# Kernel optimization log

Measured on AMD Instinct MI355X. Metric: run time of the kernel, lower is better.

## Reference

```python
import jax, jax.numpy as jnp
import numpy as np

N_NODES = 50000
N_EDGES = 200000


def _glorot(key, shape):
    fan_in, fan_out = shape[0], shape[1]
    lim = np.sqrt(6.0 / (fan_in + fan_out))
    return jax.random.uniform(key, shape, jnp.float32, -lim, lim)


def setup_inputs() -> dict:
    key = jax.random.key(0)
    ks = jax.random.split(key, 20)
    x = jax.random.normal(ks[0], (N_NODES, 2), jnp.float32)
    edge_index = jax.random.randint(ks[1], (2, N_EDGES), 0, N_NODES, jnp.int64)
    edge_attr = jax.random.uniform(ks[2], (N_EDGES, 2), jnp.float32)
    # conv1: NNConv(2 -> 32), edge nn: Linear(2,16) -> ReLU -> Linear(16, 2*32)
    nn1_w1 = _glorot(ks[3], (2, 16)); nn1_b1 = jnp.zeros((16,), jnp.float32)
    nn1_w2 = _glorot(ks[4], (16, 64)); nn1_b2 = jnp.zeros((64,), jnp.float32)
    root1 = _glorot(ks[5], (2, 32)); bias1 = jnp.zeros((32,), jnp.float32)
    # conv2: NNConv(32 -> 32), edge nn: Linear(2,16) -> ReLU -> Linear(16, 1024)
    nn2_w1 = _glorot(ks[6], (2, 16)); nn2_b1 = jnp.zeros((16,), jnp.float32)
    nn2_w2 = _glorot(ks[7], (16, 1024)); nn2_b2 = jnp.zeros((1024,), jnp.float32)
    root2 = _glorot(ks[8], (32, 32)); bias2 = jnp.zeros((32,), jnp.float32)
    # fc2: Linear(32 -> 1)  (fc1 is unused in the original forward)
    fc2_w = _glorot(ks[9], (32, 1)); fc2_b = jnp.zeros((1,), jnp.float32)
    return dict(x=x, edge_index=edge_index, edge_attr=edge_attr,
                nn1_w1=nn1_w1, nn1_b1=nn1_b1, nn1_w2=nn1_w2, nn1_b2=nn1_b2,
                root1=root1, bias1=bias1,
                nn2_w1=nn2_w1, nn2_b1=nn2_b1, nn2_w2=nn2_w2, nn2_b2=nn2_b2,
                root2=root2, bias2=bias2, fc2_w=fc2_w, fc2_b=fc2_b)


def _nnconv(x, src, dst, edge_attr, w1, b1, w2, b2, root, bias, in_ch, out_ch):
    # per-edge weight matrices from edge MLP: [E, in_ch*out_ch]
    h = jax.nn.relu(edge_attr @ w1 + b1) @ w2 + b2
    W = h.reshape(-1, in_ch, out_ch)               # [E, in, out]
    msg = jnp.einsum('ei,eio->eo', x[src], W)      # gather + per-edge matvec
    agg = jax.ops.segment_sum(msg, dst, num_segments=x.shape[0])  # scatter-add
    return agg + x @ root + bias                   # add aggr + root transform


def reference(x, edge_index, edge_attr,
              nn1_w1, nn1_b1, nn1_w2, nn1_b2, root1, bias1,
              nn2_w1, nn2_b1, nn2_w2, nn2_b2, root2, bias2,
              fc2_w, fc2_b):
    src, dst = edge_index[0], edge_index[1]
    h = jax.nn.relu(_nnconv(x, src, dst, edge_attr,
                            nn1_w1, nn1_b1, nn1_w2, nn1_b2, root1, bias1, 2, 32))
    h = jax.nn.relu(_nnconv(h, src, dst, edge_attr,
                            nn2_w1, nn2_b1, nn2_w2, nn2_b2, root2, bias2, 32, 32))
    return h @ fc2_w + fc2_b  # [N, 1]
```

## Files before the change

### kernel.cpp

```cpp
#include <hip/hip_runtime.h>


typedef __attribute__((ext_vector_type(8))) short short8;
typedef __attribute__((ext_vector_type(4))) float f32x4;

__device__ inline unsigned short f2bf(float f) {
    unsigned x = __float_as_uint(f);
    unsigned r = (x + 0x7fffu + ((x >> 16) & 1u)) >> 16;
    return (unsigned short)r;
}
__device__ inline unsigned long long pack4bf(float a, float b, float c, float d) {
    return (unsigned long long)f2bf(a) | ((unsigned long long)f2bf(b) << 16)
         | ((unsigned long long)f2bf(c) << 32) | ((unsigned long long)f2bf(d) << 48);
}

__global__ __launch_bounds__(256, 2) void edge2_mfma(
    const float* __restrict__ h1,
    const int*   __restrict__ ei,
    const float* __restrict__ ea,
    const float* __restrict__ w1,
    const float* __restrict__ b1,
    const float* __restrict__ w2,
    const float* __restrict__ b2,
    float* __restrict__ agg,
    int E)
{
    __shared__ short8 u_buf[32 * 1152 / 16];
    __shared__ short8 wrt_buf[32 * 1152 / 16];
    __shared__ int s_dst[32];
    char* u_lds = (char*)u_buf;
    char* wrt   = (char*)wrt_buf;

    const int tid = threadIdx.x;

    for (int idx = tid; idx < 32 * 544; idx += 256) {
        int o  = idx / 544;
        int kk = idx - o * 544;
        float v = (kk < 512) ? w2[(kk >> 5) * 1024 + (kk & 31) * 32 + o]
                             : b2[(kk - 512) * 32 + o];
        *(unsigned short*)(wrt + o * 1152 + kk * 2) = f2bf(v);
    }
    __syncthreads();

    const int lane = tid & 63;
    const int w    = tid >> 6;
    const int m    = w & 1;
    const int nh   = w >> 1;
    const int g16  = (lane >> 4) << 4;
    const int oo   = nh * 16 + (lane & 15);

    const char* brow = wrt + (size_t)oo * 1152;
    short8 bfrag[17];
#pragma unroll
    for (int t = 0; t < 17; ++t)
        bfrag[t] = *(const short8*)(brow + t * 64 + g16);

    float w1r0[16], w1r1[16], b1r[16];
#pragma unroll
    for (int k = 0; k < 16; ++k) {
        w1r0[k] = w1[k]; w1r1[k] = w1[16 + k]; b1r[k] = b1[k];
    }

    const int e_loc = tid >> 3, sub = tid & 7;
    const int arow_idx = m * 16 + (lane & 15);
    const char* arow = u_lds + (size_t)arow_idx * 1152;
    const unsigned axor = (unsigned)((arow_idx & 7) << 4);
    char* srow = u_lds + (size_t)e_loc * 1152;
    const unsigned sxor = (unsigned)((e_loc & 7) << 4);

    const int tiles = (E + 31) >> 5;
    for (int t0 = blockIdx.x; t0 < tiles; t0 += gridDim.x) {
        int e = t0 * 32 + e_loc;
        bool valid = e < E;
        int ec = valid ? e : 0;
        int src = ei[ec];
        if (sub == 0) s_dst[e_loc] = ei[E + ec];
        float ea0 = ea[2 * ec], ea1 = ea[2 * ec + 1];
        float4 h4 = *(const float4*)(h1 + (size_t)src * 32 + sub * 4);
        if (!valid) h4 = make_float4(0.f, 0.f, 0.f, 0.f);

        float he[16];
#pragma unroll
        for (int k = 0; k < 16; ++k) {
            float v = fmaf(ea0, w1r0[k], fmaf(ea1, w1r1[k], b1r[k]));
            he[k] = v > 0.f ? v : 0.f;
        }
#pragma unroll
        for (int k = 0; k < 16; ++k) {
            *(unsigned long long*)(srow + (((unsigned)(k * 64 + sub * 8)) ^ sxor)) =
                pack4bf(he[k] * h4.x, he[k] * h4.y, he[k] * h4.z, he[k] * h4.w);
        }
        *(unsigned long long*)(srow + (((unsigned)(1024 + sub * 8)) ^ sxor)) =
            pack4bf(h4.x, h4.y, h4.z, h4.w);
        __syncthreads();

        f32x4 acc = {0.f, 0.f, 0.f, 0.f};
#pragma unroll
        for (int t = 0; t < 17; ++t) {
            short8 a = *(const short8*)(arow + (((unsigned)(t * 64 + g16)) ^ axor));
            acc = __builtin_amdgcn_mfma_f32_16x16x32_bf16(a, bfrag[t], acc, 0, 0, 0);
        }

#pragma unroll
        for (int j = 0; j < 4; ++j) {
            int r  = ((lane >> 4) << 2) + j;
            int eg = t0 * 32 + m * 16 + r;
            if (eg < E) {
                int d = s_dst[m * 16 + r];
                atomicAdd(agg + (size_t)d * 32 + oo, acc[j]);
            }
        }
        __syncthreads();
    }
}

__global__ __launch_bounds__(256, 2) void edge1_mfma(
    const float* __restrict__ x,
    const int*   __restrict__ ei,
    const float* __restrict__ ea,
    const float* __restrict__ w1,
    const float* __restrict__ b1,
    const float* __restrict__ w2,
    const float* __restrict__ b2,
    float* __restrict__ agg,
    int E)
{
    __shared__ short8 u_buf[32 * 128 / 16];
    __shared__ short8 wrt_buf[32 * 128 / 16];
    __shared__ int s_dst[32];
    char* u_lds = (char*)u_buf;
    char* wrt   = (char*)wrt_buf;

    const int tid = threadIdx.x;

    for (int idx = tid; idx < 32 * 64; idx += 256) {
        int o = idx >> 6, kk = idx & 63;
        float v = 0.f;
        if (kk < 32)      v = w2[(kk >> 1) * 64 + (kk & 1) * 32 + o];
        else if (kk < 34) v = b2[(kk - 32) * 32 + o];
        *(unsigned short*)(wrt + o * 128 + kk * 2) = f2bf(v);
    }
    __syncthreads();

    const int lane = tid & 63;
    const int w    = tid >> 6;
    const int m    = w & 1;
    const int nh   = w >> 1;
    const int g16  = (lane >> 4) << 4;
    const int oo   = nh * 16 + (lane & 15);

    const char* brow = wrt + (size_t)oo * 128;
    short8 bfrag[2];
#pragma unroll
    for (int t = 0; t < 2; ++t)
        bfrag[t] = *(const short8*)(brow + t * 64 + g16);

    float w1r0[16], w1r1[16], b1r[16];
#pragma unroll
    for (int k = 0; k < 16; ++k) {
        w1r0[k] = w1[k]; w1r1[k] = w1[16 + k]; b1r[k] = b1[k];
    }

    const int e_loc = tid >> 3, sub = tid & 7;
    const int arow_idx = m * 16 + (lane & 15);
    const char* arow = u_lds + (size_t)arow_idx * 128;
    const unsigned axor = (unsigned)((arow_idx & 7) << 4);
    char* srow = u_lds + (size_t)e_loc * 128;
    const unsigned sxor = (unsigned)((e_loc & 7) << 4);

    const int tiles = (E + 31) >> 5;
    for (int t0 = blockIdx.x; t0 < tiles; t0 += gridDim.x) {
        int e = t0 * 32 + e_loc;
        bool valid = e < E;
        int ec = valid ? e : 0;
        int src = ei[ec];
        if (sub == 0) s_dst[e_loc] = ei[E + ec];
        float ea0 = ea[2 * ec], ea1 = ea[2 * ec + 1];
        float x0 = x[2 * src], x1 = x[2 * src + 1];
        if (!valid) { x0 = 0.f; x1 = 0.f; }

        float he[16];
#pragma unroll
        for (int k = 0; k < 16; ++k) {
            float v = fmaf(ea0, w1r0[k], fmaf(ea1, w1r1[k], b1r[k]));
            he[k] = v > 0.f ? v : 0.f;
        }
        float v8[8];
#pragma unroll
        for (int jj = 0; jj < 8; ++jj) {
            int kk = sub * 8 + jj;
            float v = 0.f;
            if (kk < 32)       v = he[kk >> 1] * ((kk & 1) ? x1 : x0);
            else if (kk == 32) v = x0;
            else if (kk == 33) v = x1;
            v8[jj] = v;
        }
        *(unsigned long long*)(srow + (((unsigned)(sub * 16)) ^ sxor)) =
            pack4bf(v8[0], v8[1], v8[2], v8[3]);
        *(unsigned long long*)(srow + (((unsigned)(sub * 16 + 8)) ^ sxor)) =
            pack4bf(v8[4], v8[5], v8[6], v8[7]);
        __syncthreads();

        f32x4 acc = {0.f, 0.f, 0.f, 0.f};
#pragma unroll
        for (int t = 0; t < 2; ++t) {
            short8 a = *(const short8*)(arow + (((unsigned)(t * 64 + g16)) ^ axor));
            acc = __builtin_amdgcn_mfma_f32_16x16x32_bf16(a, bfrag[t], acc, 0, 0, 0);
        }

#pragma unroll
        for (int j = 0; j < 4; ++j) {
            int r  = ((lane >> 4) << 2) + j;
            int eg = t0 * 32 + m * 16 + r;
            if (eg < E) {
                int d = s_dst[m * 16 + r];
                atomicAdd(agg + (size_t)d * 32 + oo, acc[j]);
            }
        }
        __syncthreads();
    }
}

__global__ __launch_bounds__(256) void node1_kernel(
    const float* __restrict__ x, const float* __restrict__ agg,
    const float* __restrict__ root, const float* __restrict__ bias,
    float* __restrict__ h1, int N)
{
    int gid = blockIdx.x * blockDim.x + threadIdx.x;
    int n = gid >> 5, o = gid & 31;
    if (n >= N) return;
    float v = agg[(size_t)n * 32 + o]
            + x[2 * n] * root[o] + x[2 * n + 1] * root[32 + o] + bias[o];
    h1[(size_t)n * 32 + o] = v > 0.f ? v : 0.f;
}

__global__ __launch_bounds__(256) void node2_kernel(
    const float* __restrict__ h1, const float* __restrict__ agg,
    const float* __restrict__ root2, const float* __restrict__ bias2,
    const float* __restrict__ fc2w, const float* __restrict__ fc2b,
    float* __restrict__ out, int N)
{
    __shared__ float s_r[1024];
    for (int t = threadIdx.x; t < 1024; t += blockDim.x) s_r[t] = root2[t];
    __syncthreads();

    int gid = blockIdx.x * blockDim.x + threadIdx.x;
    int n = gid >> 5, o = gid & 31;
    if (n >= N) return;

    float mine = h1[(size_t)n * 32 + o];
    float v = agg[(size_t)n * 32 + o] + bias2[o];
#pragma unroll
    for (int i = 0; i < 32; ++i) {
        float hi = __shfl(mine, i, 32);
        v = fmaf(hi, s_r[i * 32 + o], v);
    }
    v = v > 0.f ? v : 0.f;
    v *= fc2w[o];
#pragma unroll
    for (int off = 16; off; off >>= 1) v += __shfl_xor(v, off, 32);
    if (o == 0) out[n] = v + fc2b[0];
}

extern "C" void kernel_launch(void* const* d_in, const int* in_sizes, int n_in,
                              void* d_out, int out_size, void* d_ws, size_t ws_size,
                              hipStream_t stream) {
    const float* x      = (const float*)d_in[0];
    const int*   ei     = (const int*)  d_in[1];
    const float* ea     = (const float*)d_in[2];
    const float* nn1_w1 = (const float*)d_in[3];
    const float* nn1_b1 = (const float*)d_in[4];
    const float* nn1_w2 = (const float*)d_in[5];
    const float* nn1_b2 = (const float*)d_in[6];
    const float* root1  = (const float*)d_in[7];
    const float* bias1  = (const float*)d_in[8];
    const float* nn2_w1 = (const float*)d_in[9];
    const float* nn2_b1 = (const float*)d_in[10];
    const float* nn2_w2 = (const float*)d_in[11];
    const float* nn2_b2 = (const float*)d_in[12];
    const float* root2  = (const float*)d_in[13];
    const float* bias2  = (const float*)d_in[14];
    const float* fc2w   = (const float*)d_in[15];
    const float* fc2b   = (const float*)d_in[16];

    const int N = in_sizes[0] / 2;
    const int E = in_sizes[2] / 2;

    float* agg1 = (float*)d_ws;
    float* agg2 = agg1 + (size_t)N * 32;
    float* h1   = agg2 + (size_t)N * 32;

    hipMemsetAsync(d_ws, 0, (size_t)N * 64 * sizeof(float), stream);

    edge1_mfma<<<1024, 256, 0, stream>>>(
        x, ei, ea, nn1_w1, nn1_b1, nn1_w2, nn1_b2, agg1, E);

    node1_kernel<<<(N * 32 + 255) / 256, 256, 0, stream>>>(
        x, agg1, root1, bias1, h1, N);

    edge2_mfma<<<512, 256, 0, stream>>>(
        h1, ei, ea, nn2_w1, nn2_b1, nn2_w2, nn2_b2, agg2, E);

    node2_kernel<<<(N * 32 + 255) / 256, 256, 0, stream>>>(
        h1, agg2, root2, bias2, fc2w, fc2b, (float*)d_out, N);
}
```

Before: 193.8 us.

## Build MFMA fragments in registers, drop LDS staging and block barriers

Both edge kernels now build the A operand (edge-MLP output times gathered node features) directly in registers in MFMA fragment layout, and load the B weight fragments straight from global memory. This removes the shared-memory staging buffers and both __syncthreads per tile. The destination indices are read as an int4 per lane instead of through shared memory. Occupancy hints rise to 4 blocks per CU and edge2 launches twice as many blocks. The cost is some redundant per-lane conversion work, more register pressure from 17 fragments, and uncoalesced weight loads in the prologue.

```diff
diff --git a/kernel.cpp b/kernel.cpp
--- a/kernel.cpp
+++ b/kernel.cpp
@@ -1,20 +1,19 @@
 #include <hip/hip_runtime.h>
+#include <hip/hip_bf16.h>
 
 
 typedef __attribute__((ext_vector_type(8))) short short8;
 typedef __attribute__((ext_vector_type(4))) float f32x4;
 
-__device__ inline unsigned short f2bf(float f) {
-    unsigned x = __float_as_uint(f);
-    unsigned r = (x + 0x7fffu + ((x >> 16) & 1u)) >> 16;
-    return (unsigned short)r;
-}
-__device__ inline unsigned long long pack4bf(float a, float b, float c, float d) {
-    return (unsigned long long)f2bf(a) | ((unsigned long long)f2bf(b) << 16)
-         | ((unsigned long long)f2bf(c) << 32) | ((unsigned long long)f2bf(d) << 48);
-}
-
-__global__ __launch_bounds__(256, 2) void edge2_mfma(
+union frag_u { short8 s; unsigned u[4]; };
+
+__device__ inline unsigned cvt_pk2(float lo, float hi) {
+    union { __hip_bfloat162 h; unsigned u; } c;
+    c.h = __float22bfloat162_rn(make_float2(lo, hi));
+    return c.u;
+}
+
+__global__ __launch_bounds__(256, 4) void edge2_mfma(
     const float* __restrict__ h1,
     const int*   __restrict__ ei,
     const float* __restrict__ ea,
@@ -25,35 +24,37 @@
     float* __restrict__ agg,
     int E)
 {
-    __shared__ short8 u_buf[32 * 1152 / 16];
-    __shared__ short8 wrt_buf[32 * 1152 / 16];
-    __shared__ int s_dst[32];
-    char* u_lds = (char*)u_buf;
-    char* wrt   = (char*)wrt_buf;
-
-    const int tid = threadIdx.x;
-
-    for (int idx = tid; idx < 32 * 544; idx += 256) {
-        int o  = idx / 544;
-        int kk = idx - o * 544;
-        float v = (kk < 512) ? w2[(kk >> 5) * 1024 + (kk & 31) * 32 + o]
-                             : b2[(kk - 512) * 32 + o];
-        *(unsigned short*)(wrt + o * 1152 + kk * 2) = f2bf(v);
-    }
-    __syncthreads();
-
+    const int tid  = threadIdx.x;
     const int lane = tid & 63;
-    const int w    = tid >> 6;
-    const int m    = w & 1;
-    const int nh   = w >> 1;
-    const int g16  = (lane >> 4) << 4;
-    const int oo   = nh * 16 + (lane & 15);
-
-    const char* brow = wrt + (size_t)oo * 1152;
+    const int wv   = tid >> 6;
+    const int nh   = wv & 1;
+    const int gsel = wv >> 1;
+    const int r16  = lane & 15;
+    const int g    = lane >> 4;
+    const int oo   = nh * 16 + r16;
+    const int g8   = g * 8;
+
     short8 bfrag[17];
 #pragma unroll
-    for (int t = 0; t < 17; ++t)
-        bfrag[t] = *(const short8*)(brow + t * 64 + g16);
+    for (int t = 0; t < 16; ++t) {
+        frag_u f;
+#pragma unroll
+        for (int wd = 0; wd < 4; ++wd) {
+            int i0 = g8 + 2 * wd;
+            f.u[wd] = cvt_pk2(w2[t * 1024 + i0 * 32 + oo],
+                              w2[t * 1024 + (i0 + 1) * 32 + oo]);
+        }
+        bfrag[t] = f.s;
+    }
+    {
+        frag_u f;
+#pragma unroll
+        for (int wd = 0; wd < 4; ++wd) {
+            int i0 = g8 + 2 * wd;
+            f.u[wd] = cvt_pk2(b2[i0 * 32 + oo], b2[(i0 + 1) * 32 + oo]);
+        }
+        bfrag[16] = f.s;
+    }
 
     float w1r0[16], w1r1[16], b1r[16];
 #pragma unroll
@@ -61,60 +62,63 @@
         w1r0[k] = w1[k]; w1r1[k] = w1[16 + k]; b1r[k] = b1[k];
     }
 
-    const int e_loc = tid >> 3, sub = tid & 7;
-    const int arow_idx = m * 16 + (lane & 15);
-    const char* arow = u_lds + (size_t)arow_idx * 1152;
-    const unsigned axor = (unsigned)((arow_idx & 7) << 4);
-    char* srow = u_lds + (size_t)e_loc * 1152;
-    const unsigned sxor = (unsigned)((e_loc & 7) << 4);
-
-    const int tiles = (E + 31) >> 5;
-    for (int t0 = blockIdx.x; t0 < tiles; t0 += gridDim.x) {
-        int e = t0 * 32 + e_loc;
-        bool valid = e < E;
-        int ec = valid ? e : 0;
-        int src = ei[ec];
-        if (sub == 0) s_dst[e_loc] = ei[E + ec];
-        float ea0 = ea[2 * ec], ea1 = ea[2 * ec + 1];
-        float4 h4 = *(const float4*)(h1 + (size_t)src * 32 + sub * 4);
-        if (!valid) h4 = make_float4(0.f, 0.f, 0.f, 0.f);
+    const int pairs = (E + 31) >> 5;
+    for (int p = blockIdx.x; p < pairs; p += gridDim.x) {
+        const int base = p * 32 + gsel * 16;
+        const int edge = base + r16;
+        const bool ev = edge < E;
+        const int ec = ev ? edge : 0;
+
+        int    src = ei[ec];
+        float2 eav = *(const float2*)(ea + 2 * (size_t)ec);
+        float4 hA  = *(const float4*)(h1 + (size_t)src * 32 + g8);
+        float4 hB  = *(const float4*)(h1 + (size_t)src * 32 + g8 + 4);
+        if (!ev) { hA = make_float4(0.f,0.f,0.f,0.f); hB = make_float4(0.f,0.f,0.f,0.f); }
 
         float he[16];
 #pragma unroll
         for (int k = 0; k < 16; ++k) {
-            float v = fmaf(ea0, w1r0[k], fmaf(ea1, w1r1[k], b1r[k]));
+            float v = fmaf(eav.x, w1r0[k], fmaf(eav.y, w1r1[k], b1r[k]));
             he[k] = v > 0.f ? v : 0.f;
         }
-#pragma unroll
-        for (int k = 0; k < 16; ++k) {
-            *(unsigned long long*)(srow + (((unsigned)(k * 64 + sub * 8)) ^ sxor)) =
-                pack4bf(he[k] * h4.x, he[k] * h4.y, he[k] * h4.z, he[k] * h4.w);
-        }
-        *(unsigned long long*)(srow + (((unsigned)(1024 + sub * 8)) ^ sxor)) =
-            pack4bf(h4.x, h4.y, h4.z, h4.w);
-        __syncthreads();
 
         f32x4 acc = {0.f, 0.f, 0.f, 0.f};
 #pragma unroll
-        for (int t = 0; t < 17; ++t) {
-            short8 a = *(const short8*)(arow + (((unsigned)(t * 64 + g16)) ^ axor));
-            acc = __builtin_amdgcn_mfma_f32_16x16x32_bf16(a, bfrag[t], acc, 0, 0, 0);
-        }
-
-#pragma unroll
-        for (int j = 0; j < 4; ++j) {
-            int r  = ((lane >> 4) << 2) + j;
-            int eg = t0 * 32 + m * 16 + r;
-            if (eg < E) {
-                int d = s_dst[m * 16 + r];
-                atomicAdd(agg + (size_t)d * 32 + oo, acc[j]);
+        for (int t = 0; t < 16; ++t) {
+            frag_u a;
+            a.u[0] = cvt_pk2(he[t] * hA.x, he[t] * hA.y);
+            a.u[1] = cvt_pk2(he[t] * hA.z, he[t] * hA.w);
+            a.u[2] = cvt_pk2(he[t] * hB.x, he[t] * hB.y);
+            a.u[3] = cvt_pk2(he[t] * hB.z, he[t] * hB.w);
+            acc = __builtin_amdgcn_mfma_f32_16x16x32_bf16(a.s, bfrag[t], acc, 0, 0, 0);
+        }
+        {
+            frag_u a;
+            a.u[0] = cvt_pk2(hA.x, hA.y);
+            a.u[1] = cvt_pk2(hA.z, hA.w);
+            a.u[2] = cvt_pk2(hB.x, hB.y);
+            a.u[3] = cvt_pk2(hB.z, hB.w);
+            acc = __builtin_amdgcn_mfma_f32_16x16x32_bf16(a.s, bfrag[16], acc, 0, 0, 0);
+        }
+
+        float* ap = agg + oo;
+        if (base + g * 4 + 3 < E) {
+            int4 d4 = *(const int4*)(ei + (size_t)E + base + g * 4);
+            atomicAdd(ap + (size_t)d4.x * 32, acc[0]);
+            atomicAdd(ap + (size_t)d4.y * 32, acc[1]);
+            atomicAdd(ap + (size_t)d4.z * 32, acc[2]);
+            atomicAdd(ap + (size_t)d4.w * 32, acc[3]);
+        } else {
+#pragma unroll
+            for (int j = 0; j < 4; ++j) {
+                int eg = base + g * 4 + j;
+                if (eg < E) atomicAdd(ap + (size_t)ei[E + eg] * 32, acc[j]);
             }
         }
-        __syncthreads();
-    }
-}
-
-__global__ __launch_bounds__(256, 2) void edge1_mfma(
+    }
+}
+
+__global__ __launch_bounds__(256, 4) void edge1_mfma(
     const float* __restrict__ x,
     const int*   __restrict__ ei,
     const float* __restrict__ ea,
@@ -125,99 +129,78 @@
     float* __restrict__ agg,
     int E)
 {
-    __shared__ short8 u_buf[32 * 128 / 16];
-    __shared__ short8 wrt_buf[32 * 128 / 16];
-    __shared__ int s_dst[32];
-    char* u_lds = (char*)u_buf;
-    char* wrt   = (char*)wrt_buf;
-
-    const int tid = threadIdx.x;
-
-    for (int idx = tid; idx < 32 * 64; idx += 256) {
-        int o = idx >> 6, kk = idx & 63;
-        float v = 0.f;
-        if (kk < 32)      v = w2[(kk >> 1) * 64 + (kk & 1) * 32 + o];
-        else if (kk < 34) v = b2[(kk - 32) * 32 + o];
-        *(unsigned short*)(wrt + o * 128 + kk * 2) = f2bf(v);
-    }
-    __syncthreads();
-
+    const int tid  = threadIdx.x;
     const int lane = tid & 63;
-    const int w    = tid >> 6;
-    const int m    = w & 1;
-    const int nh   = w >> 1;
-    const int g16  = (lane >> 4) << 4;
-    const int oo   = nh * 16 + (lane & 15);
-
-    const char* brow = wrt + (size_t)oo * 128;
-    short8 bfrag[2];
-#pragma unroll
-    for (int t = 0; t < 2; ++t)
-        bfrag[t] = *(const short8*)(brow + t * 64 + g16);
-
-    float w1r0[16], w1r1[16], b1r[16];
-#pragma unroll
-    for (int k = 0; k < 16; ++k) {
-        w1r0[k] = w1[k]; w1r1[k] = w1[16 + k]; b1r[k] = b1[k];
-    }
-
-    const int e_loc = tid >> 3, sub = tid & 7;
-    const int arow_idx = m * 16 + (lane & 15);
-    const char* arow = u_lds + (size_t)arow_idx * 128;
-    const unsigned axor = (unsigned)((arow_idx & 7) << 4);
-    char* srow = u_lds + (size_t)e_loc * 128;
-    const unsigned sxor = (unsigned)((e_loc & 7) << 4);
-
-    const int tiles = (E + 31) >> 5;
-    for (int t0 = blockIdx.x; t0 < tiles; t0 += gridDim.x) {
-        int e = t0 * 32 + e_loc;
-        bool valid = e < E;
-        int ec = valid ? e : 0;
-        int src = ei[ec];
-        if (sub == 0) s_dst[e_loc] = ei[E + ec];
-        float ea0 = ea[2 * ec], ea1 = ea[2 * ec + 1];
-        float x0 = x[2 * src], x1 = x[2 * src + 1];
-        if (!valid) { x0 = 0.f; x1 = 0.f; }
-
-        float he[16];
-#pragma unroll
-        for (int k = 0; k < 16; ++k) {
-            float v = fmaf(ea0, w1r0[k], fmaf(ea1, w1r1[k], b1r[k]));
-            he[k] = v > 0.f ? v : 0.f;
-        }
-        float v8[8];
-#pragma unroll
-        for (int jj = 0; jj < 8; ++jj) {
-            int kk = sub * 8 + jj;
-            float v = 0.f;
-            if (kk < 32)       v = he[kk >> 1] * ((kk & 1) ? x1 : x0);
-            else if (kk == 32) v = x0;
-            else if (kk == 33) v = x1;
-            v8[jj] = v;
-        }
-        *(unsigned long long*)(srow + (((unsigned)(sub * 16)) ^ sxor)) =
-            pack4bf(v8[0], v8[1], v8[2], v8[3]);
-        *(unsigned long long*)(srow + (((unsigned)(sub * 16 + 8)) ^ sxor)) =
-            pack4bf(v8[4], v8[5], v8[6], v8[7]);
-        __syncthreads();
-
+    const int wv   = tid >> 6;
+    const int nh   = wv & 1;
+    const int gsel = wv >> 1;
+    const int r16  = lane & 15;
+    const int g    = lane >> 4;
+    const int oo   = nh * 16 + r16;
+    const int g8   = g * 8;
+
+    short8 bf0, bf1;
+    {
+        frag_u f;
+#pragma unroll
+        for (int wd = 0; wd < 4; ++wd) {
+            int kk0 = g8 + 2 * wd, kk1 = kk0 + 1;
+            f.u[wd] = cvt_pk2(w2[(kk0 >> 1) * 64 + (kk0 & 1) * 32 + oo],
+                              w2[(kk1 >> 1) * 64 + (kk1 & 1) * 32 + oo]);
+        }
+        bf0 = f.s;
+        f.u[0] = (g == 0) ? cvt_pk2(b2[oo], b2[32 + oo]) : 0u;
+        f.u[1] = 0u; f.u[2] = 0u; f.u[3] = 0u;
+        bf1 = f.s;
+    }
+
+    const float4 w1a = *(const float4*)(w1 + g * 4);
+    const float4 w1b = *(const float4*)(w1 + 16 + g * 4);
+    const float4 b1v = *(const float4*)(b1 + g * 4);
+
+    const int pairs = (E + 31) >> 5;
+    for (int p = blockIdx.x; p < pairs; p += gridDim.x) {
+        const int base = p * 32 + gsel * 16;
+        const int edge = base + r16;
+        const bool ev = edge < E;
+        const int ec = ev ? edge : 0;
+
+        int    src = ei[ec];
+        float2 eav = *(const float2*)(ea + 2 * (size_t)ec);
+        float2 xv  = *(const float2*)(x + 2 * (size_t)src);
+        if (!ev) xv = make_float2(0.f, 0.f);
+
+        float he0 = fmaf(eav.x, w1a.x, fmaf(eav.y, w1b.x, b1v.x)); he0 = he0 > 0.f ? he0 : 0.f;
+        float he1 = fmaf(eav.x, w1a.y, fmaf(eav.y, w1b.y, b1v.y)); he1 = he1 > 0.f ? he1 : 0.f;
+        float he2 = fmaf(eav.x, w1a.z, fmaf(eav.y, w1b.z, b1v.z)); he2 = he2 > 0.f ? he2 : 0.f;
+        float he3 = fmaf(eav.x, w1a.w, fmaf(eav.y, w1b.w, b1v.w)); he3 = he3 > 0.f ? he3 : 0.f;
+
+        frag_u a;
+        a.u[0] = cvt_pk2(he0 * xv.x, he0 * xv.y);
+        a.u[1] = cvt_pk2(he1 * xv.x, he1 * xv.y);
+        a.u[2] = cvt_pk2(he2 * xv.x, he2 * xv.y);
+        a.u[3] = cvt_pk2(he3 * xv.x, he3 * xv.y);
         f32x4 acc = {0.f, 0.f, 0.f, 0.f};
-#pragma unroll
-        for (int t = 0; t < 2; ++t) {
-            short8 a = *(const short8*)(arow + (((unsigned)(t * 64 + g16)) ^ axor));
-            acc = __builtin_amdgcn_mfma_f32_16x16x32_bf16(a, bfrag[t], acc, 0, 0, 0);
-        }
-
-#pragma unroll
-        for (int j = 0; j < 4; ++j) {
-            int r  = ((lane >> 4) << 2) + j;
-            int eg = t0 * 32 + m * 16 + r;
-            if (eg < E) {
-                int d = s_dst[m * 16 + r];
-                atomicAdd(agg + (size_t)d * 32 + oo, acc[j]);
+        acc = __builtin_amdgcn_mfma_f32_16x16x32_bf16(a.s, bf0, acc, 0, 0, 0);
+
+        a.u[0] = (g == 0) ? cvt_pk2(xv.x, xv.y) : 0u;
+        a.u[1] = 0u; a.u[2] = 0u; a.u[3] = 0u;
+        acc = __builtin_amdgcn_mfma_f32_16x16x32_bf16(a.s, bf1, acc, 0, 0, 0);
+
+        float* ap = agg + oo;
+        if (base + g * 4 + 3 < E) {
+            int4 d4 = *(const int4*)(ei + (size_t)E + base + g * 4);
+            atomicAdd(ap + (size_t)d4.x * 32, acc[0]);
+            atomicAdd(ap + (size_t)d4.y * 32, acc[1]);
+            atomicAdd(ap + (size_t)d4.z * 32, acc[2]);
+            atomicAdd(ap + (size_t)d4.w * 32, acc[3]);
+        } else {
+#pragma unroll
+            for (int j = 0; j < 4; ++j) {
+                int eg = base + g * 4 + j;
+                if (eg < E) atomicAdd(ap + (size_t)ei[E + eg] * 32, acc[j]);
             }
         }
-        __syncthreads();
     }
 }
 
@@ -298,7 +281,7 @@
     node1_kernel<<<(N * 32 + 255) / 256, 256, 0, stream>>>(
         x, agg1, root1, bias1, h1, N);
 
-    edge2_mfma<<<512, 256, 0, stream>>>(
+    edge2_mfma<<<1024, 256, 0, stream>>>(
         h1, ei, ea, nn2_w1, nn2_b1, nn2_w2, nn2_b2, agg2, E);
 
     node2_kernel<<<(N * 32 + 255) / 256, 256, 0, stream>>>(
```

Result: faster. 169.9 us (-12.3%).
